# Kernel tuning notes

Hardware: AMD Instinct MI355X
Metric: run time of the kernel (lower is better)

## Reference

```python
import jax, jax.numpy as jnp
import numpy as np

EPS = 1e-5  # nn.LayerNorm default eps


def setup_inputs() -> dict:
    key = jax.random.key(0)
    k1, k2, k3, k4 = jax.random.split(key, 4)
    B, S, HS, N = 4, 8192, 1024, 4
    x = jax.random.normal(k1, (B, S, HS), dtype=jnp.float32)
    alpha = jax.random.uniform(k2, (B, S, N), dtype=jnp.float32)
    W = jax.random.normal(k3, (N, HS), dtype=jnp.float32)
    b = jax.random.normal(k4, (N, HS), dtype=jnp.float32)
    return {"x": x, "alpha": alpha, "W": W, "b": b}


def reference(x, alpha, W, b):
    # All anchors normalize the same x, so compute the normalization once.
    mean = jnp.mean(x, axis=-1, keepdims=True)
    var = jnp.mean(jnp.square(x - mean), axis=-1, keepdims=True)  # biased, as in torch LayerNorm
    xhat = (x - mean) * jax.lax.rsqrt(var + EPS)  # [B, S, HS]
    # alpha-weighted mixture of per-anchor affine params:
    # out = sum_n alpha_n * (xhat * W_n + b_n) = xhat * (alpha @ W) + (alpha @ b)
    eff_w = jnp.einsum('bsn,nh->bsh', alpha, W)
    eff_b = jnp.einsum('bsn,nh->bsh', alpha, b)
    return xhat * eff_w + eff_b
```

## Files before the change

### kernel.cpp

```cpp
#include <hip/hip_runtime.h>


constexpr int HS = 1024;

typedef float vfloat4 __attribute__((ext_vector_type(4)));

__device__ __forceinline__ float4 ld4(const float* p) {
    return *reinterpret_cast<const float4*>(p);
}

__device__ __forceinline__ void st4_nt(float* p, float a, float b, float c, float d) {
    vfloat4 v = {a, b, c, d};
    __builtin_nontemporal_store(v, reinterpret_cast<vfloat4*>(p));
}

template <int CTRL>
__device__ __forceinline__ float dpp_add(float x) {
    int y = __builtin_amdgcn_update_dpp(0, __float_as_int(x), CTRL, 0xf, 0xf, true);
    return x + __int_as_float(y);
}

__device__ __forceinline__ float wave_sum_to_lane63(float x) {
    x = dpp_add<0x111>(x);
    x = dpp_add<0x112>(x);
    x = dpp_add<0x114>(x);
    x = dpp_add<0x118>(x);
    x = dpp_add<0x142>(x);
    x = dpp_add<0x143>(x);
    return x;
}

__global__ __launch_bounds__(256, 8) void lns_kernel(
    const float* __restrict__ x,
    const float* __restrict__ alpha,
    const float* __restrict__ W,
    const float* __restrict__ Bias,
    float* __restrict__ out,
    int nrows)
{
    const int t = threadIdx.x;
    const int h4 = t * 4;

    const float4 w0 = ld4(W + 0 * HS + h4);
    const float4 w1 = ld4(W + 1 * HS + h4);
    const float4 w2 = ld4(W + 2 * HS + h4);
    const float4 w3 = ld4(W + 3 * HS + h4);
    const float4 b0 = ld4(Bias + 0 * HS + h4);
    const float4 b1 = ld4(Bias + 1 * HS + h4);
    const float4 b2 = ld4(Bias + 2 * HS + h4);
    const float4 b3 = ld4(Bias + 3 * HS + h4);

    __shared__ vfloat4 red[2][4];

    const int wv = t >> 6;
    int iter = 0;

    for (int row = blockIdx.x * 2; row < nrows; row += gridDim.x * 2, ++iter) {
        const size_t base0 = (size_t)row * HS + h4;
        const size_t base1 = base0 + HS;

        const float4 x0 = ld4(x + base0);
        const float4 x1 = ld4(x + base1);
        const float4 a0 = ld4(alpha + (size_t)row * 4);
        const float4 a1 = ld4(alpha + (size_t)row * 4 + 4);

        float s0  = (x0.x + x0.y) + (x0.z + x0.w);
        float ss0 = fmaf(x0.x, x0.x, fmaf(x0.y, x0.y, fmaf(x0.z, x0.z, x0.w * x0.w)));
        float s1  = (x1.x + x1.y) + (x1.z + x1.w);
        float ss1 = fmaf(x1.x, x1.x, fmaf(x1.y, x1.y, fmaf(x1.z, x1.z, x1.w * x1.w)));

        s0  = wave_sum_to_lane63(s0);
        ss0 = wave_sum_to_lane63(ss0);
        s1  = wave_sum_to_lane63(s1);
        ss1 = wave_sum_to_lane63(ss1);

        const int p = iter & 1;
        if ((t & 63) == 63) {
            vfloat4 v = {s0, ss0, s1, ss1};
            red[p][wv] = v;
        }
        __syncthreads();

        const vfloat4 r0 = red[p][0];
        const vfloat4 r1 = red[p][1];
        const vfloat4 r2 = red[p][2];
        const vfloat4 r3 = red[p][3];
        s0  = (r0.x + r1.x) + (r2.x + r3.x);
        ss0 = (r0.y + r1.y) + (r2.y + r3.y);
        s1  = (r0.z + r1.z) + (r2.z + r3.z);
        ss1 = (r0.w + r1.w) + (r2.w + r3.w);

        const float mean0 = s0 * (1.0f / HS);
        const float var0  = fmaf(-mean0, mean0, ss0 * (1.0f / HS));
        const float rstd0 = rsqrtf(var0 + 1e-5f);
        const float mean1 = s1 * (1.0f / HS);
        const float var1  = fmaf(-mean1, mean1, ss1 * (1.0f / HS));
        const float rstd1 = rsqrtf(var1 + 1e-5f);

        float o0x, o0y, o0z, o0w, o1x, o1y, o1z, o1w;
        {
            float ew, eb;
            ew = fmaf(a0.x, w0.x, fmaf(a0.y, w1.x, fmaf(a0.z, w2.x, a0.w * w3.x)));
            eb = fmaf(a0.x, b0.x, fmaf(a0.y, b1.x, fmaf(a0.z, b2.x, a0.w * b3.x)));
            o0x = fmaf((x0.x - mean0) * rstd0, ew, eb);
            ew = fmaf(a0.x, w0.y, fmaf(a0.y, w1.y, fmaf(a0.z, w2.y, a0.w * w3.y)));
            eb = fmaf(a0.x, b0.y, fmaf(a0.y, b1.y, fmaf(a0.z, b2.y, a0.w * b3.y)));
            o0y = fmaf((x0.y - mean0) * rstd0, ew, eb);
            ew = fmaf(a0.x, w0.z, fmaf(a0.y, w1.z, fmaf(a0.z, w2.z, a0.w * w3.z)));
            eb = fmaf(a0.x, b0.z, fmaf(a0.y, b1.z, fmaf(a0.z, b2.z, a0.w * b3.z)));
            o0z = fmaf((x0.z - mean0) * rstd0, ew, eb);
            ew = fmaf(a0.x, w0.w, fmaf(a0.y, w1.w, fmaf(a0.z, w2.w, a0.w * w3.w)));
            eb = fmaf(a0.x, b0.w, fmaf(a0.y, b1.w, fmaf(a0.z, b2.w, a0.w * b3.w)));
            o0w = fmaf((x0.w - mean0) * rstd0, ew, eb);

            ew = fmaf(a1.x, w0.x, fmaf(a1.y, w1.x, fmaf(a1.z, w2.x, a1.w * w3.x)));
            eb = fmaf(a1.x, b0.x, fmaf(a1.y, b1.x, fmaf(a1.z, b2.x, a1.w * b3.x)));
            o1x = fmaf((x1.x - mean1) * rstd1, ew, eb);
            ew = fmaf(a1.x, w0.y, fmaf(a1.y, w1.y, fmaf(a1.z, w2.y, a1.w * w3.y)));
            eb = fmaf(a1.x, b0.y, fmaf(a1.y, b1.y, fmaf(a1.z, b2.y, a1.w * b3.y)));
            o1y = fmaf((x1.y - mean1) * rstd1, ew, eb);
            ew = fmaf(a1.x, w0.z, fmaf(a1.y, w1.z, fmaf(a1.z, w2.z, a1.w * w3.z)));
            eb = fmaf(a1.x, b0.z, fmaf(a1.y, b1.z, fmaf(a1.z, b2.z, a1.w * b3.z)));
            o1z = fmaf((x1.z - mean1) * rstd1, ew, eb);
            ew = fmaf(a1.x, w0.w, fmaf(a1.y, w1.w, fmaf(a1.z, w2.w, a1.w * w3.w)));
            eb = fmaf(a1.x, b0.w, fmaf(a1.y, b1.w, fmaf(a1.z, b2.w, a1.w * b3.w)));
            o1w = fmaf((x1.w - mean1) * rstd1, ew, eb);
        }

        st4_nt(out + base0, o0x, o0y, o0z, o0w);
        st4_nt(out + base1, o1x, o1y, o1z, o1w);
    }
}

extern "C" void kernel_launch(void* const* d_in, const int* in_sizes, int n_in,
                              void* d_out, int out_size, void* d_ws, size_t ws_size,
                              hipStream_t stream) {
    const float* x     = (const float*)d_in[0];
    const float* alpha = (const float*)d_in[1];
    const float* W     = (const float*)d_in[2];
    const float* Bias  = (const float*)d_in[3];
    float* out = (float*)d_out;

    const int nrows = in_sizes[0] / HS;

    const int grid = 2048;
    lns_kernel<<<grid, 256, 0, stream>>>(x, alpha, W, Bias, out, nrows);
}
```

Measured before the change: 46.58 us.

## Process four rows per block with register double-buffered prefetch of next rows

Each block now handles four rows per iteration and loads the next iteration's x and alpha into registers before computing the current rows. This overlaps global loads with the reduction and the output math. The grid is halved and the occupancy hint lowered to accommodate the higher register use. The iteration count uses floor division, so rows beyond a multiple of grid*4 would be skipped, and there is no bounds check on the initial prefetch.

```diff
diff --git a/kernel.cpp b/kernel.cpp
--- a/kernel.cpp
+++ b/kernel.cpp
@@ -1,7 +1,8 @@
 #include <hip/hip_runtime.h>
 
 
-constexpr int HS = 1024;
+constexpr int HS  = 1024;
+constexpr int BPI = 4;
 
 typedef float vfloat4 __attribute__((ext_vector_type(4)));
 
@@ -30,7 +31,28 @@
     return x;
 }
 
-__global__ __launch_bounds__(256, 8) void lns_kernel(
+#define SUMS(xv, s, ss)                                                        \
+    float s  = (xv.x + xv.y) + (xv.z + xv.w);                                  \
+    float ss = fmaf(xv.x, xv.x, fmaf(xv.y, xv.y, fmaf(xv.z, xv.z, xv.w * xv.w)));
+
+#define EMIT(xv, av, mean, rstd, dst) do {                                     \
+    float ew, eb, o0, o1, o2, o3;                                              \
+    ew = fmaf(av.x, w0.x, fmaf(av.y, w1.x, fmaf(av.z, w2.x, av.w * w3.x)));    \
+    eb = fmaf(av.x, b0.x, fmaf(av.y, b1.x, fmaf(av.z, b2.x, av.w * b3.x)));    \
+    o0 = fmaf((xv.x - mean) * rstd, ew, eb);                                   \
+    ew = fmaf(av.x, w0.y, fmaf(av.y, w1.y, fmaf(av.z, w2.y, av.w * w3.y)));    \
+    eb = fmaf(av.x, b0.y, fmaf(av.y, b1.y, fmaf(av.z, b2.y, av.w * b3.y)));    \
+    o1 = fmaf((xv.y - mean) * rstd, ew, eb);                                   \
+    ew = fmaf(av.x, w0.z, fmaf(av.y, w1.z, fmaf(av.z, w2.z, av.w * w3.z)));    \
+    eb = fmaf(av.x, b0.z, fmaf(av.y, b1.z, fmaf(av.z, b2.z, av.w * b3.z)));    \
+    o2 = fmaf((xv.z - mean) * rstd, ew, eb);                                   \
+    ew = fmaf(av.x, w0.w, fmaf(av.y, w1.w, fmaf(av.z, w2.w, av.w * w3.w)));    \
+    eb = fmaf(av.x, b0.w, fmaf(av.y, b1.w, fmaf(av.z, b2.w, av.w * b3.w)));    \
+    o3 = fmaf((xv.w - mean) * rstd, ew, eb);                                   \
+    st4_nt(dst, o0, o1, o2, o3);                                               \
+} while (0)
+
+__global__ __launch_bounds__(256, 4) void lns_kernel(
     const float* __restrict__ x,
     const float* __restrict__ alpha,
     const float* __restrict__ W,
@@ -38,7 +60,7 @@
     float* __restrict__ out,
     int nrows)
 {
-    const int t = threadIdx.x;
+    const int t  = threadIdx.x;
     const int h4 = t * 4;
 
     const float4 w0 = ld4(W + 0 * HS + h4);
@@ -50,85 +72,91 @@
     const float4 b2 = ld4(Bias + 2 * HS + h4);
     const float4 b3 = ld4(Bias + 3 * HS + h4);
 
-    __shared__ vfloat4 red[2][4];
+    __shared__ vfloat4 red[2][4][2];
 
-    const int wv = t >> 6;
-    int iter = 0;
+    const int wv     = t >> 6;
+    const int stride = gridDim.x * BPI;
+    const int iters  = nrows / stride;
+    int row          = blockIdx.x * BPI;
 
-    for (int row = blockIdx.x * 2; row < nrows; row += gridDim.x * 2, ++iter) {
-        const size_t base0 = (size_t)row * HS + h4;
-        const size_t base1 = base0 + HS;
+    size_t base = (size_t)row * HS + h4;
+    float4 xc0 = ld4(x + base);
+    float4 xc1 = ld4(x + base + HS);
+    float4 xc2 = ld4(x + base + 2 * HS);
+    float4 xc3 = ld4(x + base + 3 * HS);
+    const float* ap = alpha + (size_t)row * 4;
+    float4 aA = ld4(ap);
+    float4 aB = ld4(ap + 4);
+    float4 aC = ld4(ap + 8);
+    float4 aD = ld4(ap + 12);
 
-        const float4 x0 = ld4(x + base0);
-        const float4 x1 = ld4(x + base1);
-        const float4 a0 = ld4(alpha + (size_t)row * 4);
-        const float4 a1 = ld4(alpha + (size_t)row * 4 + 4);
+    for (int it = 0; it < iters; ++it, row += stride) {
+        float4 xn0, xn1, xn2, xn3, nA, nB, nC, nD;
+        const bool more = (it + 1 < iters);
+        if (more) {
+            const size_t nb = (size_t)(row + stride) * HS + h4;
+            xn0 = ld4(x + nb);
+            xn1 = ld4(x + nb + HS);
+            xn2 = ld4(x + nb + 2 * HS);
+            xn3 = ld4(x + nb + 3 * HS);
+            const float* np = alpha + (size_t)(row + stride) * 4;
+            nA = ld4(np);
+            nB = ld4(np + 4);
+            nC = ld4(np + 8);
+            nD = ld4(np + 12);
+        }
 
-        float s0  = (x0.x + x0.y) + (x0.z + x0.w);
-        float ss0 = fmaf(x0.x, x0.x, fmaf(x0.y, x0.y, fmaf(x0.z, x0.z, x0.w * x0.w)));
-        float s1  = (x1.x + x1.y) + (x1.z + x1.w);
-        float ss1 = fmaf(x1.x, x1.x, fmaf(x1.y, x1.y, fmaf(x1.z, x1.z, x1.w * x1.w)));
+        SUMS(xc0, s0, ss0);
+        SUMS(xc1, s1, ss1);
+        SUMS(xc2, s2, ss2);
+        SUMS(xc3, s3, ss3);
 
         s0  = wave_sum_to_lane63(s0);
         ss0 = wave_sum_to_lane63(ss0);
         s1  = wave_sum_to_lane63(s1);
         ss1 = wave_sum_to_lane63(ss1);
+        s2  = wave_sum_to_lane63(s2);
+        ss2 = wave_sum_to_lane63(ss2);
+        s3  = wave_sum_to_lane63(s3);
+        ss3 = wave_sum_to_lane63(ss3);
 
-        const int p = iter & 1;
+        const int p = it & 1;
         if ((t & 63) == 63) {
-            vfloat4 v = {s0, ss0, s1, ss1};
-            red[p][wv] = v;
+            vfloat4 u = {s0, ss0, s1, ss1};
+            vfloat4 v = {s2, ss2, s3, ss3};
+            red[p][wv][0] = u;
+            red[p][wv][1] = v;
         }
         __syncthreads();
 
-        const vfloat4 r0 = red[p][0];
-        const vfloat4 r1 = red[p][1];
-        const vfloat4 r2 = red[p][2];
-        const vfloat4 r3 = red[p][3];
-        s0  = (r0.x + r1.x) + (r2.x + r3.x);
-        ss0 = (r0.y + r1.y) + (r2.y + r3.y);
-        s1  = (r0.z + r1.z) + (r2.z + r3.z);
-        ss1 = (r0.w + r1.w) + (r2.w + r3.w);
+        const vfloat4 u0 = red[p][0][0], u1 = red[p][1][0], u2 = red[p][2][0], u3 = red[p][3][0];
+        const vfloat4 v0 = red[p][0][1], v1 = red[p][1][1], v2 = red[p][2][1], v3 = red[p][3][1];
+        s0  = (u0.x + u1.x) + (u2.x + u3.x);
+        ss0 = (u0.y + u1.y) + (u2.y + u3.y);
+        s1  = (u0.z + u1.z) + (u2.z + u3.z);
+        ss1 = (u0.w + u1.w) + (u2.w + u3.w);
+        s2  = (v0.x + v1.x) + (v2.x + v3.x);
+        ss2 = (v0.y + v1.y) + (v2.y + v3.y);
+        s3  = (v0.z + v1.z) + (v2.z + v3.z);
+        ss3 = (v0.w + v1.w) + (v2.w + v3.w);
 
         const float mean0 = s0 * (1.0f / HS);
-        const float var0  = fmaf(-mean0, mean0, ss0 * (1.0f / HS));
-        const float rstd0 = rsqrtf(var0 + 1e-5f);
+        const float rstd0 = rsqrtf(fmaf(-mean0, mean0, ss0 * (1.0f / HS)) + 1e-5f);
         const float mean1 = s1 * (1.0f / HS);
-        const float var1  = fmaf(-mean1, mean1, ss1 * (1.0f / HS));
-        const float rstd1 = rsqrtf(var1 + 1e-5f);
+        const float rstd1 = rsqrtf(fmaf(-mean1, mean1, ss1 * (1.0f / HS)) + 1e-5f);
+        const float mean2 = s2 * (1.0f / HS);
+        const float rstd2 = rsqrtf(fmaf(-mean2, mean2, ss2 * (1.0f / HS)) + 1e-5f);
+        const float mean3 = s3 * (1.0f / HS);
+        const float rstd3 = rsqrtf(fmaf(-mean3, mean3, ss3 * (1.0f / HS)) + 1e-5f);
 
-        float o0x, o0y, o0z, o0w, o1x, o1y, o1z, o1w;
-        {
-            float ew, eb;
-            ew = fmaf(a0.x, w0.x, fmaf(a0.y, w1.x, fmaf(a0.z, w2.x, a0.w * w3.x)));
-            eb = fmaf(a0.x, b0.x, fmaf(a0.y, b1.x, fmaf(a0.z, b2.x, a0.w * b3.x)));
-            o0x = fmaf((x0.x - mean0) * rstd0, ew, eb);
-            ew = fmaf(a0.x, w0.y, fmaf(a0.y, w1.y, fmaf(a0.z, w2.y, a0.w * w3.y)));
-            eb = fmaf(a0.x, b0.y, fmaf(a0.y, b1.y, fmaf(a0.z, b2.y, a0.w * b3.y)));
-            o0y = fmaf((x0.y - mean0) * rstd0, ew, eb);
-            ew = fmaf(a0.x, w0.z, fmaf(a0.y, w1.z, fmaf(a0.z, w2.z, a0.w * w3.z)));
-            eb = fmaf(a0.x, b0.z, fmaf(a0.y, b1.z, fmaf(a0.z, b2.z, a0.w * b3.z)));
-            o0z = fmaf((x0.z - mean0) * rstd0, ew, eb);
-            ew = fmaf(a0.x, w0.w, fmaf(a0.y, w1.w, fmaf(a0.z, w2.w, a0.w * w3.w)));
-            eb = fmaf(a0.x, b0.w, fmaf(a0.y, b1.w, fmaf(a0.z, b2.w, a0.w * b3.w)));
-            o0w = fmaf((x0.w - mean0) * rstd0, ew, eb);
+        base = (size_t)row * HS + h4;
+        EMIT(xc0, aA, mean0, rstd0, out + base);
+        EMIT(xc1, aB, mean1, rstd1, out + base + HS);
+        EMIT(xc2, aC, mean2, rstd2, out + base + 2 * HS);
+        EMIT(xc3, aD, mean3, rstd3, out + base + 3 * HS);
 
-            ew = fmaf(a1.x, w0.x, fmaf(a1.y, w1.x, fmaf(a1.z, w2.x, a1.w * w3.x)));
-            eb = fmaf(a1.x, b0.x, fmaf(a1.y, b1.x, fmaf(a1.z, b2.x, a1.w * b3.x)));
-            o1x = fmaf((x1.x - mean1) * rstd1, ew, eb);
-            ew = fmaf(a1.x, w0.y, fmaf(a1.y, w1.y, fmaf(a1.z, w2.y, a1.w * w3.y)));
-            eb = fmaf(a1.x, b0.y, fmaf(a1.y, b1.y, fmaf(a1.z, b2.y, a1.w * b3.y)));
-            o1y = fmaf((x1.y - mean1) * rstd1, ew, eb);
-            ew = fmaf(a1.x, w0.z, fmaf(a1.y, w1.z, fmaf(a1.z, w2.z, a1.w * w3.z)));
-            eb = fmaf(a1.x, b0.z, fmaf(a1.y, b1.z, fmaf(a1.z, b2.z, a1.w * b3.z)));
-            o1z = fmaf((x1.z - mean1) * rstd1, ew, eb);
-            ew = fmaf(a1.x, w0.w, fmaf(a1.y, w1.w, fmaf(a1.z, w2.w, a1.w * w3.w)));
-            eb = fmaf(a1.x, b0.w, fmaf(a1.y, b1.w, fmaf(a1.z, b2.w, a1.w * b3.w)));
-            o1w = fmaf((x1.w - mean1) * rstd1, ew, eb);
-        }
-
-        st4_nt(out + base0, o0x, o0y, o0z, o0w);
-        st4_nt(out + base1, o1x, o1y, o1z, o1w);
+        xc0 = xn0; xc1 = xn1; xc2 = xn2; xc3 = xn3;
+        aA = nA; aB = nB; aC = nC; aD = nD;
     }
 }
 
@@ -143,6 +171,6 @@
 
     const int nrows = in_sizes[0] / HS;
 
-    const int grid = 2048;
+    const int grid = 1024;
     lns_kernel<<<grid, 256, 0, stream>>>(x, alpha, W, Bias, out, nrows);
 }
```

Result: no change. 46.29 us, median of 2 (-0.6%).
